# Kernel optimization log

Hardware: AMD Instinct MI355X
Metric: run time of the kernel (lower is better)

The kernel has to match this reference:

```python
import jax, jax.numpy as jnp
import numpy as np

B, N, E, ED, H, HID, OUT = 128, 100, 3200, 8, 4, 16, 32


def _ln(x, g, b):
    m = x.mean(-1, keepdims=True)
    v = ((x - m) ** 2).mean(-1, keepdims=True)
    return (x - m) / jnp.sqrt(v + 1e-5) * g + b


def _seg_softmax(logits, seg, n):
    # logits: [Etot, H], seg: [Etot] target node ids
    m = jax.ops.segment_max(logits, seg, num_segments=n)
    ex = jnp.exp(logits - m[seg])
    s = jax.ops.segment_sum(ex, seg, num_segments=n)
    return ex / (s[seg] + 1e-16)


def _tconv(x, src, dst, ea, Wq, bq, Wk, bk, Wv, bv, We, Ws, bs, heads, ch, n):
    # PyG TransformerConv, concat=False, root_weight=True, beta=False
    q = (x @ Wq.T + bq).reshape(-1, heads, ch)
    k = (x @ Wk.T + bk).reshape(-1, heads, ch)
    v = (x @ Wv.T + bv).reshape(-1, heads, ch)
    e = (ea @ We.T).reshape(-1, heads, ch)
    alpha = (q[dst] * (k[src] + e)).sum(-1) / jnp.sqrt(jnp.float32(ch))  # [Etot,H]
    alpha = _seg_softmax(alpha, dst, n)
    msg = (v[src] + e) * alpha[..., None]
    out = jax.ops.segment_sum(msg, dst, num_segments=n)  # [n,H,ch]
    out = out.mean(axis=1)  # concat=False -> head mean
    return out + x @ Ws.T + bs


def setup_inputs() -> dict:
    key = jax.random.key(0)
    ks = jax.random.split(key, 32)
    d = {}
    d['nodes_feats'] = jax.random.randint(ks[0], (B, N, 1), 0, 5).astype(jnp.float32)
    d['edge_index'] = jax.random.randint(ks[1], (B, 2, E), 0, N).astype(jnp.int32)
    d['edge_attr'] = jax.random.normal(ks[2], (B, E, ED), jnp.float32)
    d['agent_id'] = jax.random.randint(ks[3], (B, 1), 0, N).astype(jnp.int32)
    s = 0.1
    d['entity_embed'] = jax.random.normal(ks[4], (5, 4), jnp.float32)
    d['W1'] = jax.random.normal(ks[5], (HID, 4 + ED), jnp.float32) * s
    d['b1'] = jnp.zeros((HID,), jnp.float32)
    d['W2'] = jax.random.normal(ks[6], (HID, HID), jnp.float32) * s
    d['b2'] = jnp.zeros((HID,), jnp.float32)
    d['W3'] = jax.random.normal(ks[7], (HID, HID), jnp.float32) * s
    d['b3'] = jnp.zeros((HID,), jnp.float32)
    d['ln_g'] = jnp.ones((HID,), jnp.float32)
    d['ln_b'] = jnp.zeros((HID,), jnp.float32)
    i = 8
    for pre, ch, outd in (('g1', HID, HID), ('g2', OUT, OUT)):
        d[pre + '_Wq'] = jax.random.normal(ks[i + 0], (H * ch, HID), jnp.float32) * s
        d[pre + '_bq'] = jnp.zeros((H * ch,), jnp.float32)
        d[pre + '_Wk'] = jax.random.normal(ks[i + 1], (H * ch, HID), jnp.float32) * s
        d[pre + '_bk'] = jnp.zeros((H * ch,), jnp.float32)
        d[pre + '_Wv'] = jax.random.normal(ks[i + 2], (H * ch, HID), jnp.float32) * s
        d[pre + '_bv'] = jnp.zeros((H * ch,), jnp.float32)
        d[pre + '_We'] = jax.random.normal(ks[i + 3], (H * ch, ED), jnp.float32) * s
        d[pre + '_Ws'] = jax.random.normal(ks[i + 4], (outd, HID), jnp.float32) * s
        d[pre + '_bs'] = jnp.zeros((outd,), jnp.float32)
        i += 5
    return d


def reference(nodes_feats, edge_index, edge_attr, agent_id, entity_embed,
              W1, b1, W2, b2, W3, b3, ln_g, ln_b,
              g1_Wq, g1_bq, g1_Wk, g1_bk, g1_Wv, g1_bv, g1_We, g1_Ws, g1_bs,
              g2_Wq, g2_bq, g2_Wk, g2_bk, g2_Wv, g2_bv, g2_We, g2_Ws, g2_bs):
    n_tot = B * N
    # batched graph -> flat graph with per-batch node offsets
    offs = (jnp.arange(B, dtype=edge_index.dtype) * N)[:, None, None]
    ei = (edge_index + offs).transpose(1, 0, 2).reshape(2, -1)  # [2, B*E]
    src, dst = ei[0], ei[1]
    x = nodes_feats.reshape(-1, 1)            # [n_tot, 1]
    ea = edge_attr.reshape(-1, ED)            # [B*E, ED]

    # Embedding message-passing layer (aggr='add')
    etype = x[:, 0].astype(jnp.int32)[src]
    emb = entity_embed[etype]                  # [Etot, 4]
    h = jnp.concatenate([emb, ea], axis=1)
    h = _ln(jax.nn.relu(h @ W1.T + b1), ln_g, ln_b)
    h = _ln(jax.nn.relu(h @ W2.T + b2), ln_g, ln_b)
    h = _ln(jax.nn.relu(h @ W3.T + b3), ln_g, ln_b)
    z = jax.ops.segment_sum(h, dst, num_segments=n_tot)  # [n_tot, 16]

    a = _tconv(z, src, dst, ea, g1_Wq, g1_bq, g1_Wk, g1_bk, g1_Wv, g1_bv,
               g1_We, g1_Ws, g1_bs, H, HID, n_tot)
    a = _tconv(a, src, dst, ea, g2_Wq, g2_bq, g2_Wk, g2_bk, g2_Wv, g2_bv,
               g2_We, g2_Ws, g2_bs, H, OUT, n_tot)
    a = jax.nn.relu(a).reshape(B, N, OUT)
    # graph_aggr == 'agent': gather the agent node per batch
    out = jnp.take_along_axis(a, agent_id[:, :, None].astype(jnp.int32), axis=1)
    return out[:, 0, :]  # [B, OUT]
```

## Files before the change

### kernel.cpp

```cpp
#include <hip/hip_runtime.h>
#include <math.h>
#include <stdint.h>

#define Bb   128
#define Nn   100
#define Ee   3200
#define NTOT (Bb*Nn)
#define ETOT (Bb*Ee)



__global__ __launch_bounds__(256) void k_zero(int* __restrict__ p) {
    int i = blockIdx.x * 256 + threadIdx.x;
    if (i < 2 * NTOT) p[i] = 0;
}

__global__ __launch_bounds__(256) void k_count(const int* __restrict__ ei, int* __restrict__ pos) {
    int ge = (blockIdx.x & 7) * (ETOT / 8) + (blockIdx.x >> 3) * 256 + threadIdx.x;
    int b = ge / Ee;
    int e = ge - b * Ee;
    int dst = ei[b * 2 * Ee + Ee + e] + b * Nn;
    atomicAdd(&pos[dst], 1);
}

__global__ __launch_bounds__(256) void k_scan(int* __restrict__ pos, int* __restrict__ off) {
    __shared__ int part[256];
    int t = threadIdx.x;
    const int per = NTOT / 256;
    int s = 0;
#pragma unroll
    for (int j = 0; j < per; j++) s += pos[t * per + j];
    part[t] = s;
    __syncthreads();
    for (int d = 1; d < 256; d <<= 1) {
        int v = (t >= d) ? part[t - d] : 0;
        __syncthreads();
        part[t] += v;
        __syncthreads();
    }
    int run = (t > 0) ? part[t - 1] : 0;
    for (int j = 0; j < per; j++) {
        int i = t * per + j;
        int cval = pos[i];
        off[i] = run;
        pos[i] = run;
        run += cval;
    }
    if (t == 255) off[NTOT] = run;
}

__global__ __launch_bounds__(256) void k_fill(const int* __restrict__ ei, int* __restrict__ pos,
                                              int2* __restrict__ cpair) {
    int ge = (blockIdx.x & 7) * (ETOT / 8) + (blockIdx.x >> 3) * 256 + threadIdx.x;
    int b = ge / Ee;
    int e = ge - b * Ee;
    int src = ei[b * 2 * Ee + e] + b * Nn;
    int dst = ei[b * 2 * Ee + Ee + e] + b * Nn;
    int idx = atomicAdd(&pos[dst], 1);
    cpair[idx] = make_int2(src, ge);
}


__global__ __launch_bounds__(64) void k_mark(const int* __restrict__ agent,
                                             const int* __restrict__ off,
                                             const int2* __restrict__ cpair,
                                             int* __restrict__ mark) {
    int b = ((blockIdx.x & 7) << 4) + (blockIdx.x >> 3);
    int lane = threadIdx.x;
    int n = b * Nn + agent[b];
    if (lane == 0) mark[n] = 1;
    int o0 = off[n];
    int deg = off[n + 1] - o0;
    for (int i = lane; i < deg; i += 64) mark[cpair[o0 + i].x] = 1;
}


__device__ __forceinline__ void ln_reg(float* h, const float* __restrict__ g,
                                       const float* __restrict__ b) {
    float s = 0.f;
#pragma unroll
    for (int c = 0; c < 16; c++) s += h[c];
    float m = s * 0.0625f;
    float v = 0.f;
#pragma unroll
    for (int c = 0; c < 16; c++) { float d = h[c] - m; v += d * d; }
    float r = rsqrtf(v * 0.0625f + 1e-5f);
#pragma unroll
    for (int c = 0; c < 16; c++) h[c] = (h[c] - m) * r * g[c] + b[c];
}

__global__ __launch_bounds__(256) void k_mlp(
    const float* __restrict__ nf, const float* __restrict__ ea, const float* __restrict__ ee,
    const float* __restrict__ W1, const float* __restrict__ b1,
    const float* __restrict__ W2, const float* __restrict__ b2,
    const float* __restrict__ W3, const float* __restrict__ b3,
    const float* __restrict__ lg, const float* __restrict__ lb,
    const int2* __restrict__ cpair,
    float* __restrict__ h)
{
    int t = (blockIdx.x & 7) * (ETOT / 8) + (blockIdx.x >> 3) * 256 + threadIdx.x;
    int2 p = cpair[t];
    int src = p.x, ge = p.y;
    int et = (int)nf[src];

    float in[12];
#pragma unroll
    for (int j = 0; j < 4; j++) in[j] = ee[et * 4 + j];
    const float4* ea4 = (const float4*)(ea + (size_t)ge * 8);
    float4 ua = ea4[0], ub = ea4[1];
    in[4] = ua.x; in[5] = ua.y; in[6] = ua.z; in[7] = ua.w;
    in[8] = ub.x; in[9] = ub.y; in[10] = ub.z; in[11] = ub.w;

    float h1[16];
#pragma unroll
    for (int c = 0; c < 16; c++) {
        float s = b1[c];
#pragma unroll
        for (int j = 0; j < 12; j++) s = fmaf(W1[c * 12 + j], in[j], s);
        h1[c] = fmaxf(s, 0.f);
    }
    ln_reg(h1, lg, lb);

    float h2[16];
#pragma unroll
    for (int c = 0; c < 16; c++) {
        float s = b2[c];
#pragma unroll
        for (int j = 0; j < 16; j++) s = fmaf(W2[c * 16 + j], h1[j], s);
        h2[c] = fmaxf(s, 0.f);
    }
    ln_reg(h2, lg, lb);

    float h3[16];
#pragma unroll
    for (int c = 0; c < 16; c++) {
        float s = b3[c];
#pragma unroll
        for (int j = 0; j < 16; j++) s = fmaf(W3[c * 16 + j], h2[j], s);
        h3[c] = fmaxf(s, 0.f);
    }
    ln_reg(h3, lg, lb);

    float4* hp = (float4*)(h + (size_t)t * 16);
    hp[0] = make_float4(h3[0], h3[1], h3[2], h3[3]);
    hp[1] = make_float4(h3[4], h3[5], h3[6], h3[7]);
    hp[2] = make_float4(h3[8], h3[9], h3[10], h3[11]);
    hp[3] = make_float4(h3[12], h3[13], h3[14], h3[15]);
}


__global__ __launch_bounds__(256) void k_zsum(
    const float* __restrict__ h,
    const float* __restrict__ Wq, const float* __restrict__ bq,
    const float* __restrict__ Wk, const float* __restrict__ bk,
    const float* __restrict__ Wv, const float* __restrict__ bv,
    const int* __restrict__ off,
    float* __restrict__ z, float* __restrict__ q1, float* __restrict__ k1, float* __restrict__ v1)
{
    int lane = threadIdx.x & 63;
    int wid  = threadIdx.x >> 6;
    int n    = (blockIdx.x & 7) * (NTOT / 8) + (blockIdx.x >> 3) * 4 + wid;
    int c    = lane & 15;
    int slot = lane >> 4;

    int o0 = off[n];
    int deg = off[n + 1] - o0;

    float zp = 0.f;
    for (int base = 0; base < deg; base += 4) {
        int i = base + slot;
        float v = 0.f;
        if (i < deg) v = h[(size_t)(o0 + i) * 16 + c];
        zp += v;
    }
    zp += __shfl_xor(zp, 16);
    zp += __shfl_xor(zp, 32);

    if (lane < 16) z[n * 16 + lane] = zp;

    float aq = bq[lane], ak = bk[lane], av = bv[lane];
#pragma unroll
    for (int j = 0; j < 16; j++) {
        float zj = __shfl(zp, j, 16);
        aq = fmaf(Wq[lane * 16 + j], zj, aq);
        ak = fmaf(Wk[lane * 16 + j], zj, ak);
        av = fmaf(Wv[lane * 16 + j], zj, av);
    }
    q1[n * 64 + lane] = aq;
    k1[n * 64 + lane] = ak;
    v1[n * 64 + lane] = av;
}


__global__ __launch_bounds__(256) void k_attn1(
    const float* __restrict__ ea,
    const float* __restrict__ q1, const float* __restrict__ k1, const float* __restrict__ v1,
    const float* __restrict__ We, const float* __restrict__ Ws, const float* __restrict__ bs,
    const float* __restrict__ z, const int* __restrict__ mark,
    const int* __restrict__ off, const int2* __restrict__ cpair,
    float* __restrict__ a1)
{
    int lane = threadIdx.x & 63;
    int wid  = threadIdx.x >> 6;
    int n    = (blockIdx.x & 7) * (NTOT / 8) + (blockIdx.x >> 3) * 4 + wid;

    if (!mark[n]) return;

    float wer[8];
#pragma unroll
    for (int j = 0; j < 8; j++) wer[j] = We[lane * 8 + j];
    float ql = q1[n * 64 + lane];

    int o0 = off[n];
    int deg = off[n + 1] - o0;

    float m = -1e30f, l = 0.f, acc = 0.f;
    int i = 0;
    for (; i + 2 <= deg; i += 2) {
        int2 pA = cpair[o0 + i];
        int2 pB = cpair[o0 + i + 1];
        const float4* eaA = (const float4*)(ea + (size_t)pA.y * 8);
        const float4* eaB = (const float4*)(ea + (size_t)pB.y * 8);
        float4 a0v = eaA[0], a1v = eaA[1], b0v = eaB[0], b1v = eaB[1];
        float eA = wer[0] * a0v.x + wer[1] * a0v.y + wer[2] * a0v.z + wer[3] * a0v.w
                 + wer[4] * a1v.x + wer[5] * a1v.y + wer[6] * a1v.z + wer[7] * a1v.w;
        float eB = wer[0] * b0v.x + wer[1] * b0v.y + wer[2] * b0v.z + wer[3] * b0v.w
                 + wer[4] * b1v.x + wer[5] * b1v.y + wer[6] * b1v.z + wer[7] * b1v.w;
        float kA = k1[(size_t)pA.x * 64 + lane];
        float kB = k1[(size_t)pB.x * 64 + lane];
        float vA = v1[(size_t)pA.x * 64 + lane];
        float vB = v1[(size_t)pB.x * 64 + lane];
        float tA = ql * (kA + eA);
        float tB = ql * (kB + eB);
        tA += __shfl_xor(tA, 1, 16);  tB += __shfl_xor(tB, 1, 16);
        tA += __shfl_xor(tA, 2, 16);  tB += __shfl_xor(tB, 2, 16);
        tA += __shfl_xor(tA, 4, 16);  tB += __shfl_xor(tB, 4, 16);
        tA += __shfl_xor(tA, 8, 16);  tB += __shfl_xor(tB, 8, 16);
        float lA = tA * 0.25f;
        float lB = tB * 0.25f;
        float nm = fmaxf(m, fmaxf(lA, lB));
        float sc = __expf(m - nm);
        float wA = __expf(lA - nm);
        float wB = __expf(lB - nm);
        acc = acc * sc + wA * (vA + eA) + wB * (vB + eB);
        l   = l * sc + wA + wB;
        m   = nm;
    }
    for (; i < deg; i++) {
        int2 p = cpair[o0 + i];
        const float4* ea4 = (const float4*)(ea + (size_t)p.y * 8);
        float4 u0 = ea4[0], u1 = ea4[1];
        float el = wer[0] * u0.x + wer[1] * u0.y + wer[2] * u0.z + wer[3] * u0.w
                 + wer[4] * u1.x + wer[5] * u1.y + wer[6] * u1.z + wer[7] * u1.w;
        float kl = k1[(size_t)p.x * 64 + lane];
        float t = ql * (kl + el);
        t += __shfl_xor(t, 1, 16);
        t += __shfl_xor(t, 2, 16);
        t += __shfl_xor(t, 4, 16);
        t += __shfl_xor(t, 8, 16);
        float logit = t * 0.25f;
        float nm = fmaxf(m, logit);
        float sc = __expf(m - nm);
        float w  = __expf(logit - nm);
        float vl = v1[(size_t)p.x * 64 + lane];
        acc = acc * sc + w * (vl + el);
        l   = l * sc + w;
        m   = nm;
    }
    float y = (deg > 0) ? (acc / l) : 0.f;
    y += __shfl_xor(y, 16);
    y += __shfl_xor(y, 32);
    y *= 0.25f;

    if (lane < 16) {
        float r = bs[lane];
#pragma unroll
        for (int j = 0; j < 16; j++) r = fmaf(Ws[lane * 16 + j], z[n * 16 + j], r);
        a1[n * 16 + lane] = y + r;
    }
}


__global__ __launch_bounds__(256) void k_g2(
    const float* __restrict__ ea, const float* __restrict__ a1, const int* __restrict__ agent,
    const float* __restrict__ Wq, const float* __restrict__ bq,
    const float* __restrict__ Wk, const float* __restrict__ bk,
    const float* __restrict__ Wv, const float* __restrict__ bv,
    const float* __restrict__ We, const float* __restrict__ Ws, const float* __restrict__ bs,
    const int* __restrict__ off, const int2* __restrict__ cpair,
    float* __restrict__ out)
{
    __shared__ float sm[4][64], sl[4][64], sa0[4][64], sa1[4][64];
    int b = ((blockIdx.x & 7) << 4) + (blockIdx.x >> 3);
    int lane = threadIdx.x & 63;
    int w = threadIdx.x >> 6;
    int n = b * Nn + agent[b];
    int v0 = lane * 2, v1i = lane * 2 + 1;

    float aa[16];
#pragma unroll
    for (int j = 0; j < 16; j++) aa[j] = a1[n * 16 + j];

    float wk0[16], wk1[16], wv0[16], wv1[16], we0[8], we1[8];
#pragma unroll
    for (int j = 0; j < 16; j++) {
        wk0[j] = Wk[v0 * 16 + j];  wk1[j] = Wk[v1i * 16 + j];
        wv0[j] = Wv[v0 * 16 + j];  wv1[j] = Wv[v1i * 16 + j];
    }
#pragma unroll
    for (int j = 0; j < 8; j++) { we0[j] = We[v0 * 8 + j]; we1[j] = We[v1i * 8 + j]; }

    float q0 = bq[v0], q1v = bq[v1i];
#pragma unroll
    for (int j = 0; j < 16; j++) {
        q0  = fmaf(Wq[v0 * 16 + j],  aa[j], q0);
        q1v = fmaf(Wq[v1i * 16 + j], aa[j], q1v);
    }

    int o0 = off[n];
    int deg = off[n + 1] - o0;

    float m = -1e30f, l = 0.f, a0 = 0.f, a1c = 0.f;
    for (int i = w; i < deg; i += 4) {
        int2 p = cpair[o0 + i];
        int src = p.x, ge = p.y;
        float as[16];
#pragma unroll
        for (int j = 0; j < 16; j++) as[j] = a1[src * 16 + j];
        const float4* ea4 = (const float4*)(ea + (size_t)ge * 8);
        float4 u0 = ea4[0], u1 = ea4[1];
        float eav[8] = {u0.x, u0.y, u0.z, u0.w, u1.x, u1.y, u1.z, u1.w};

        float k0 = bk[v0], k1v = bk[v1i], vv0 = bv[v0], vv1 = bv[v1i];
#pragma unroll
        for (int j = 0; j < 16; j++) {
            k0  = fmaf(wk0[j], as[j], k0);
            k1v = fmaf(wk1[j], as[j], k1v);
            vv0 = fmaf(wv0[j], as[j], vv0);
            vv1 = fmaf(wv1[j], as[j], vv1);
        }
        float e0 = 0.f, e1 = 0.f;
#pragma unroll
        for (int j = 0; j < 8; j++) { e0 = fmaf(we0[j], eav[j], e0); e1 = fmaf(we1[j], eav[j], e1); }

        float t = q0 * (k0 + e0) + q1v * (k1v + e1);
        t += __shfl_xor(t, 1, 16);
        t += __shfl_xor(t, 2, 16);
        t += __shfl_xor(t, 4, 16);
        t += __shfl_xor(t, 8, 16);
        float logit = t * 0.17677669529663687f;
        float nm = fmaxf(m, logit);
        float sc = __expf(m - nm);
        float wgt = __expf(logit - nm);
        a0  = a0 * sc + wgt * (vv0 + e0);
        a1c = a1c * sc + wgt * (vv1 + e1);
        l   = l * sc + wgt;
        m   = nm;
    }
    sm[w][lane] = m; sl[w][lane] = l; sa0[w][lane] = a0; sa1[w][lane] = a1c;
    __syncthreads();
    if (w == 0) {
        float M = fmaxf(fmaxf(sm[0][lane], sm[1][lane]), fmaxf(sm[2][lane], sm[3][lane]));
        float L = 0.f, A0 = 0.f, A1 = 0.f;
#pragma unroll
        for (int ww = 0; ww < 4; ww++) {
            float sc = __expf(sm[ww][lane] - M);
            L  += sc * sl[ww][lane];
            A0 += sc * sa0[ww][lane];
            A1 += sc * sa1[ww][lane];
        }
        float y0 = (deg > 0) ? (A0 / L) : 0.f;
        float y1 = (deg > 0) ? (A1 / L) : 0.f;
        y0 += __shfl_xor(y0, 16); y0 += __shfl_xor(y0, 32);
        y1 += __shfl_xor(y1, 16); y1 += __shfl_xor(y1, 32);
        y0 *= 0.25f; y1 *= 0.25f;

        if (lane < 16) {
            int c0 = lane * 2, c1 = lane * 2 + 1;
            float r0 = bs[c0], r1 = bs[c1];
#pragma unroll
            for (int j = 0; j < 16; j++) {
                r0 = fmaf(Ws[c0 * 16 + j], aa[j], r0);
                r1 = fmaf(Ws[c1 * 16 + j], aa[j], r1);
            }
            out[b * 32 + c0] = fmaxf(y0 + r0, 0.f);
            out[b * 32 + c1] = fmaxf(y1 + r1, 0.f);
        }
    }
}


extern "C" void kernel_launch(void* const* d_in, const int* in_sizes, int n_in,
                              void* d_out, int out_size, void* d_ws, size_t ws_size,
                              hipStream_t stream) {
    (void)in_sizes; (void)n_in; (void)out_size; (void)ws_size;
    const float* nf    = (const float*)d_in[0];
    const int*   ei    = (const int*)d_in[1];
    const float* ea    = (const float*)d_in[2];
    const int*   agent = (const int*)d_in[3];
    const float* ee    = (const float*)d_in[4];
    const float* W1    = (const float*)d_in[5];
    const float* b1    = (const float*)d_in[6];
    const float* W2    = (const float*)d_in[7];
    const float* b2    = (const float*)d_in[8];
    const float* W3    = (const float*)d_in[9];
    const float* b3    = (const float*)d_in[10];
    const float* lg    = (const float*)d_in[11];
    const float* lb    = (const float*)d_in[12];
    const float* g1Wq  = (const float*)d_in[13];
    const float* g1bq  = (const float*)d_in[14];
    const float* g1Wk  = (const float*)d_in[15];
    const float* g1bk  = (const float*)d_in[16];
    const float* g1Wv  = (const float*)d_in[17];
    const float* g1bv  = (const float*)d_in[18];
    const float* g1We  = (const float*)d_in[19];
    const float* g1Ws  = (const float*)d_in[20];
    const float* g1bs  = (const float*)d_in[21];
    const float* g2Wq  = (const float*)d_in[22];
    const float* g2bq  = (const float*)d_in[23];
    const float* g2Wk  = (const float*)d_in[24];
    const float* g2bk  = (const float*)d_in[25];
    const float* g2Wv  = (const float*)d_in[26];
    const float* g2bv  = (const float*)d_in[27];
    const float* g2We  = (const float*)d_in[28];
    const float* g2Ws  = (const float*)d_in[29];
    const float* g2bs  = (const float*)d_in[30];
    float* out = (float*)d_out;

    char* w = (char*)d_ws;
    int* pos   = (int*)w;  w += (size_t)NTOT * 4;
    int* mark  = (int*)w;  w += (size_t)NTOT * 4;
    int* off   = (int*)w;  w += (size_t)(NTOT + 4) * 4;
    w = (char*)(((uintptr_t)w + 15) & ~(uintptr_t)15);
    int2* cpair = (int2*)w; w += (size_t)ETOT * 8;
    float* h   = (float*)w; w += (size_t)ETOT * 16 * 4;
    float* z   = (float*)w; w += (size_t)NTOT * 16 * 4;
    float* q1  = (float*)w; w += (size_t)NTOT * 64 * 4;
    float* k1  = (float*)w; w += (size_t)NTOT * 64 * 4;
    float* v1  = (float*)w; w += (size_t)NTOT * 64 * 4;
    float* a1  = (float*)w; w += (size_t)NTOT * 16 * 4;

    k_zero<<<dim3((2 * NTOT + 255) / 256), dim3(256), 0, stream>>>(pos);
    k_count<<<dim3(ETOT / 256), dim3(256), 0, stream>>>(ei, pos);
    k_scan<<<dim3(1), dim3(256), 0, stream>>>(pos, off);
    k_fill<<<dim3(ETOT / 256), dim3(256), 0, stream>>>(ei, pos, cpair);
    k_mark<<<dim3(Bb), dim3(64), 0, stream>>>(agent, off, cpair, mark);
    k_mlp<<<dim3(ETOT / 256), dim3(256), 0, stream>>>(
        nf, ea, ee, W1, b1, W2, b2, W3, b3, lg, lb, cpair, h);
    k_zsum<<<dim3(NTOT / 4), dim3(256), 0, stream>>>(
        h, g1Wq, g1bq, g1Wk, g1bk, g1Wv, g1bv, off, z, q1, k1, v1);
    k_attn1<<<dim3(NTOT / 4), dim3(256), 0, stream>>>(
        ea, q1, k1, v1, g1We, g1Ws, g1bs, z, mark, off, cpair, a1);
    k_g2<<<dim3(Bb), dim3(256), 0, stream>>>(
        ea, a1, agent, g2Wq, g2bq, g2Wk, g2bk, g2Wv, g2bv, g2We, g2Ws, g2bs,
        off, cpair, out);
}
```

Baseline: 240.9 us.

## Build per-graph CSR in one kernel and fuse edge MLP into node sum

The five CSR-building kernels (zero, count, global scan, fill, mark) are replaced by one block-per-graph kernel that counts, scans and fills using shared-memory atomics, and marks the agent's neighbours directly from the edge list. The per-edge MLP is fused into the node-aggregation kernel: each wave computes the MLP for its node's incoming edges and reduces them through shared memory, so the ETOT x 16 intermediate h buffer is never written or read. This removes several launches, a serial single-block scan and a large round trip through global memory. In exchange, MLP work in each block is padded to the largest degree among its four nodes, and the CSR stage runs only 128 blocks.

After: 204.6 us. 15.1% less time.

```diff
diff --git a/kernel.cpp b/kernel.cpp
--- a/kernel.cpp
+++ b/kernel.cpp
@@ -10,68 +10,48 @@
 
 
 
-__global__ __launch_bounds__(256) void k_zero(int* __restrict__ p) {
-    int i = blockIdx.x * 256 + threadIdx.x;
-    if (i < 2 * NTOT) p[i] = 0;
-}
-
-__global__ __launch_bounds__(256) void k_count(const int* __restrict__ ei, int* __restrict__ pos) {
-    int ge = (blockIdx.x & 7) * (ETOT / 8) + (blockIdx.x >> 3) * 256 + threadIdx.x;
-    int b = ge / Ee;
-    int e = ge - b * Ee;
-    int dst = ei[b * 2 * Ee + Ee + e] + b * Nn;
-    atomicAdd(&pos[dst], 1);
-}
-
-__global__ __launch_bounds__(256) void k_scan(int* __restrict__ pos, int* __restrict__ off) {
-    __shared__ int part[256];
+__global__ __launch_bounds__(256) void k_csr(const int* __restrict__ ei,
+                                             const int* __restrict__ agent,
+                                             int* __restrict__ off,
+                                             int2* __restrict__ cpair,
+                                             int* __restrict__ mark)
+{
+    int b = ((blockIdx.x & 7) << 4) + (blockIdx.x >> 3);
     int t = threadIdx.x;
-    const int per = NTOT / 256;
-    int s = 0;
-#pragma unroll
-    for (int j = 0; j < per; j++) s += pos[t * per + j];
-    part[t] = s;
-    __syncthreads();
-    for (int d = 1; d < 256; d <<= 1) {
-        int v = (t >= d) ? part[t - d] : 0;
+    __shared__ int cnt[128];
+    __shared__ int exc[128];
+    __shared__ int cur[128];
+    if (t < 128) cnt[t] = 0;
+    if (t < Nn) mark[b * Nn + t] = 0;
+    __syncthreads();
+    const int* eis = ei + (size_t)b * 2 * Ee;
+    const int* eid = eis + Ee;
+    for (int e = t; e < Ee; e += 256) atomicAdd(&cnt[eid[e]], 1);
+    __syncthreads();
+    if (t < 128) exc[t] = cnt[t];
+    __syncthreads();
+    for (int d = 1; d < 128; d <<= 1) {
+        int v = 0;
+        if (t < 128 && t >= d) v = exc[t - d];
         __syncthreads();
-        part[t] += v;
+        if (t < 128) exc[t] += v;
         __syncthreads();
     }
-    int run = (t > 0) ? part[t - 1] : 0;
-    for (int j = 0; j < per; j++) {
-        int i = t * per + j;
-        int cval = pos[i];
-        off[i] = run;
-        pos[i] = run;
-        run += cval;
-    }
-    if (t == 255) off[NTOT] = run;
-}
-
-__global__ __launch_bounds__(256) void k_fill(const int* __restrict__ ei, int* __restrict__ pos,
-                                              int2* __restrict__ cpair) {
-    int ge = (blockIdx.x & 7) * (ETOT / 8) + (blockIdx.x >> 3) * 256 + threadIdx.x;
-    int b = ge / Ee;
-    int e = ge - b * Ee;
-    int src = ei[b * 2 * Ee + e] + b * Nn;
-    int dst = ei[b * 2 * Ee + Ee + e] + b * Nn;
-    int idx = atomicAdd(&pos[dst], 1);
-    cpair[idx] = make_int2(src, ge);
-}
-
-
-__global__ __launch_bounds__(64) void k_mark(const int* __restrict__ agent,
-                                             const int* __restrict__ off,
-                                             const int2* __restrict__ cpair,
-                                             int* __restrict__ mark) {
-    int b = ((blockIdx.x & 7) << 4) + (blockIdx.x >> 3);
-    int lane = threadIdx.x;
-    int n = b * Nn + agent[b];
-    if (lane == 0) mark[n] = 1;
-    int o0 = off[n];
-    int deg = off[n + 1] - o0;
-    for (int i = lane; i < deg; i += 64) mark[cpair[o0 + i].x] = 1;
+    if (t < 128) { int e0 = exc[t] - cnt[t]; exc[t] = e0; cur[t] = e0; }
+    __syncthreads();
+    if (t < Nn) off[b * Nn + t] = b * Ee + exc[t];
+    if (b == Bb - 1 && t == 0) off[NTOT] = ETOT;
+    for (int e = t; e < Ee; e += 256) {
+        int dst = eid[e];
+        int idx = atomicAdd(&cur[dst], 1);
+        cpair[b * Ee + idx] = make_int2(eis[e] + b * Nn, b * Ee + e);
+    }
+    int an = agent[b];
+    __syncthreads();
+    if (t == 0) mark[b * Nn + an] = 1;
+    for (int e = t; e < Ee; e += 256) {
+        if (eid[e] == an) mark[b * Nn + eis[e]] = 1;
+    }
 }
 
 
@@ -89,92 +69,88 @@
     for (int c = 0; c < 16; c++) h[c] = (h[c] - m) * r * g[c] + b[c];
 }
 
-__global__ __launch_bounds__(256) void k_mlp(
+__global__ __launch_bounds__(256) void k_mlpz(
     const float* __restrict__ nf, const float* __restrict__ ea, const float* __restrict__ ee,
     const float* __restrict__ W1, const float* __restrict__ b1,
     const float* __restrict__ W2, const float* __restrict__ b2,
     const float* __restrict__ W3, const float* __restrict__ b3,
     const float* __restrict__ lg, const float* __restrict__ lb,
-    const int2* __restrict__ cpair,
-    float* __restrict__ h)
-{
-    int t = (blockIdx.x & 7) * (ETOT / 8) + (blockIdx.x >> 3) * 256 + threadIdx.x;
-    int2 p = cpair[t];
-    int src = p.x, ge = p.y;
-    int et = (int)nf[src];
-
-    float in[12];
-#pragma unroll
-    for (int j = 0; j < 4; j++) in[j] = ee[et * 4 + j];
-    const float4* ea4 = (const float4*)(ea + (size_t)ge * 8);
-    float4 ua = ea4[0], ub = ea4[1];
-    in[4] = ua.x; in[5] = ua.y; in[6] = ua.z; in[7] = ua.w;
-    in[8] = ub.x; in[9] = ub.y; in[10] = ub.z; in[11] = ub.w;
-
-    float h1[16];
-#pragma unroll
-    for (int c = 0; c < 16; c++) {
-        float s = b1[c];
-#pragma unroll
-        for (int j = 0; j < 12; j++) s = fmaf(W1[c * 12 + j], in[j], s);
-        h1[c] = fmaxf(s, 0.f);
-    }
-    ln_reg(h1, lg, lb);
-
-    float h2[16];
-#pragma unroll
-    for (int c = 0; c < 16; c++) {
-        float s = b2[c];
-#pragma unroll
-        for (int j = 0; j < 16; j++) s = fmaf(W2[c * 16 + j], h1[j], s);
-        h2[c] = fmaxf(s, 0.f);
-    }
-    ln_reg(h2, lg, lb);
-
-    float h3[16];
-#pragma unroll
-    for (int c = 0; c < 16; c++) {
-        float s = b3[c];
-#pragma unroll
-        for (int j = 0; j < 16; j++) s = fmaf(W3[c * 16 + j], h2[j], s);
-        h3[c] = fmaxf(s, 0.f);
-    }
-    ln_reg(h3, lg, lb);
-
-    float4* hp = (float4*)(h + (size_t)t * 16);
-    hp[0] = make_float4(h3[0], h3[1], h3[2], h3[3]);
-    hp[1] = make_float4(h3[4], h3[5], h3[6], h3[7]);
-    hp[2] = make_float4(h3[8], h3[9], h3[10], h3[11]);
-    hp[3] = make_float4(h3[12], h3[13], h3[14], h3[15]);
-}
-
-
-__global__ __launch_bounds__(256) void k_zsum(
-    const float* __restrict__ h,
     const float* __restrict__ Wq, const float* __restrict__ bq,
     const float* __restrict__ Wk, const float* __restrict__ bk,
     const float* __restrict__ Wv, const float* __restrict__ bv,
-    const int* __restrict__ off,
+    const int* __restrict__ off, const int2* __restrict__ cpair,
     float* __restrict__ z, float* __restrict__ q1, float* __restrict__ k1, float* __restrict__ v1)
 {
+    __shared__ float hs[4][64][17];
+    __shared__ int sdeg[4];
     int lane = threadIdx.x & 63;
     int wid  = threadIdx.x >> 6;
     int n    = (blockIdx.x & 7) * (NTOT / 8) + (blockIdx.x >> 3) * 4 + wid;
-    int c    = lane & 15;
-    int slot = lane >> 4;
 
     int o0 = off[n];
     int deg = off[n + 1] - o0;
+    if (lane == 0) sdeg[wid] = deg;
+    __syncthreads();
+    int mdeg = max(max(sdeg[0], sdeg[1]), max(sdeg[2], sdeg[3]));
+    int chunks = (mdeg + 63) >> 6;
 
     float zp = 0.f;
-    for (int base = 0; base < deg; base += 4) {
-        int i = base + slot;
-        float v = 0.f;
-        if (i < deg) v = h[(size_t)(o0 + i) * 16 + c];
-        zp += v;
-    }
-    zp += __shfl_xor(zp, 16);
-    zp += __shfl_xor(zp, 32);
+    for (int ch = 0; ch < chunks; ch++) {
+        int i = ch * 64 + lane;
+        float h3[16];
+        if (i < deg) {
+            int2 p = cpair[o0 + i];
+            int et = (int)nf[p.x];
+            float in[12];
+#pragma unroll
+            for (int j = 0; j < 4; j++) in[j] = ee[et * 4 + j];
+            const float4* ea4 = (const float4*)(ea + (size_t)p.y * 8);
+            float4 ua = ea4[0], ub = ea4[1];
+            in[4] = ua.x; in[5] = ua.y; in[6] = ua.z; in[7] = ua.w;
+            in[8] = ub.x; in[9] = ub.y; in[10] = ub.z; in[11] = ub.w;
+
+            float h1[16];
+#pragma unroll
+            for (int c = 0; c < 16; c++) {
+                float s = b1[c];
+#pragma unroll
+                for (int j = 0; j < 12; j++) s = fmaf(W1[c * 12 + j], in[j], s);
+                h1[c] = fmaxf(s, 0.f);
+            }
+            ln_reg(h1, lg, lb);
+            float h2[16];
+#pragma unroll
+            for (int c = 0; c < 16; c++) {
+                float s = b2[c];
+#pragma unroll
+                for (int j = 0; j < 16; j++) s = fmaf(W2[c * 16 + j], h1[j], s);
+                h2[c] = fmaxf(s, 0.f);
+            }
+            ln_reg(h2, lg, lb);
+#pragma unroll
+            for (int c = 0; c < 16; c++) {
+                float s = b3[c];
+#pragma unroll
+                for (int j = 0; j < 16; j++) s = fmaf(W3[c * 16 + j], h2[j], s);
+                h3[c] = fmaxf(s, 0.f);
+            }
+            ln_reg(h3, lg, lb);
+        } else {
+#pragma unroll
+            for (int c = 0; c < 16; c++) h3[c] = 0.f;
+        }
+#pragma unroll
+        for (int c = 0; c < 16; c++) hs[wid][lane][c] = h3[c];
+        __syncthreads();
+        int g = lane >> 4, c = lane & 15;
+        float s = 0.f;
+#pragma unroll
+        for (int k = 0; k < 16; k++) s += hs[wid][g * 16 + k][c];
+        s += __shfl_xor(s, 16);
+        s += __shfl_xor(s, 32);
+        zp += s;
+        __syncthreads();
+    }
 
     if (lane < 16) z[n * 16 + lane] = zp;
 
@@ -428,27 +404,21 @@
     float* out = (float*)d_out;
 
     char* w = (char*)d_ws;
-    int* pos   = (int*)w;  w += (size_t)NTOT * 4;
     int* mark  = (int*)w;  w += (size_t)NTOT * 4;
     int* off   = (int*)w;  w += (size_t)(NTOT + 4) * 4;
     w = (char*)(((uintptr_t)w + 15) & ~(uintptr_t)15);
     int2* cpair = (int2*)w; w += (size_t)ETOT * 8;
-    float* h   = (float*)w; w += (size_t)ETOT * 16 * 4;
     float* z   = (float*)w; w += (size_t)NTOT * 16 * 4;
     float* q1  = (float*)w; w += (size_t)NTOT * 64 * 4;
     float* k1  = (float*)w; w += (size_t)NTOT * 64 * 4;
     float* v1  = (float*)w; w += (size_t)NTOT * 64 * 4;
     float* a1  = (float*)w; w += (size_t)NTOT * 16 * 4;
 
-    k_zero<<<dim3((2 * NTOT + 255) / 256), dim3(256), 0, stream>>>(pos);
-    k_count<<<dim3(ETOT / 256), dim3(256), 0, stream>>>(ei, pos);
-    k_scan<<<dim3(1), dim3(256), 0, stream>>>(pos, off);
-    k_fill<<<dim3(ETOT / 256), dim3(256), 0, stream>>>(ei, pos, cpair);
-    k_mark<<<dim3(Bb), dim3(64), 0, stream>>>(agent, off, cpair, mark);
-    k_mlp<<<dim3(ETOT / 256), dim3(256), 0, stream>>>(
-        nf, ea, ee, W1, b1, W2, b2, W3, b3, lg, lb, cpair, h);
-    k_zsum<<<dim3(NTOT / 4), dim3(256), 0, stream>>>(
-        h, g1Wq, g1bq, g1Wk, g1bk, g1Wv, g1bv, off, z, q1, k1, v1);
+    k_csr<<<dim3(Bb), dim3(256), 0, stream>>>(ei, agent, off, cpair, mark);
+    k_mlpz<<<dim3(NTOT / 4), dim3(256), 0, stream>>>(
+        nf, ea, ee, W1, b1, W2, b2, W3, b3, lg, lb,
+        g1Wq, g1bq, g1Wk, g1bk, g1Wv, g1bv,
+        off, cpair, z, q1, k1, v1);
     k_attn1<<<dim3(NTOT / 4), dim3(256), 0, stream>>>(
         ea, q1, k1, v1, g1We, g1Ws, g1bs, z, mark, off, cpair, a1);
     k_g2<<<dim3(Bb), dim3(256), 0, stream>>>(
```
